# Kernel tuning notes

Hardware: AMD Instinct MI355X
Metric: run time of the kernel (lower is better)

Reference implementation:

```python
import jax, jax.numpy as jnp
import numpy as np

N_NODES = 100000
N_EDGES = 6400000
N_HEADS = 8


def setup_inputs() -> dict:
    key = jax.random.key(0)
    k1, k2 = jax.random.split(key)
    edge_val = jax.random.normal(k1, (N_EDGES, N_HEADS), dtype=jnp.float32)
    row = jax.random.randint(k2, (N_EDGES,), 0, N_NODES, dtype=jnp.int64)
    return {"edge_val": edge_val, "row": row, "num_nodes": N_NODES}


def reference(edge_val, row, num_nodes):
    # Per-head rescale: torch halves edge_val until max <= 10.
    # Halving k times == multiply by 0.5**k with k = ceil(log2(max/10)) when max > 10.
    m = jnp.max(edge_val, axis=0)  # [H]
    k = jnp.where(m > 10.0, jnp.ceil(jnp.log2(jnp.maximum(m, 1e-30) / 10.0)), 0.0)
    k = jnp.maximum(k, 0.0)
    scale = jnp.power(jnp.float32(0.5), jax.lax.stop_gradient(k))  # [H]
    e = jnp.exp(edge_val * scale)  # [E, H]
    # Per-destination-node sum of exp values (spmm of ones == segment sum by row)
    node_sum = jax.ops.segment_sum(e, row, num_segments=num_nodes)  # [N, H]
    return e / node_sum[row]  # [E, H]
```

## Files before the change

kernel.cpp:

```cpp
#include <hip/hip_runtime.h>

#define NHEADS 8
#define NNODES 100000
#define SLICE_NODES 500
#define NSLICES 200
#define NCHUNK 16
#define NBLK2 512
#define SEGCAP 128
#define SEGPC (NBLK2 / NCHUNK)
#define SLICE_F (SLICE_NODES * NHEADS)
#define SIDX_CAP 3072
#define WS_NSUM_OFF 1024

typedef float f32x4 __attribute__((ext_vector_type(4)));

#define PAIRS_B ((size_t)NBLK2 * NSLICES * SEGCAP * 4)
#define PART_B ((size_t)NSLICES * NCHUNK * SLICE_F * 4)

__device__ __forceinline__ unsigned fenc(float f) {
    unsigned u = __float_as_uint(f);
    return (u & 0x80000000u) ? ~u : (u | 0x80000000u);
}
__device__ __forceinline__ float fdec(unsigned u) {
    unsigned b = (u & 0x80000000u) ? (u ^ 0x80000000u) : ~u;
    return __uint_as_float(b);
}

__global__ void kinit(unsigned* __restrict__ gmax) {
    if (threadIdx.x < NHEADS) gmax[threadIdx.x] = 0u;
}

__global__ void __launch_bounds__(512) kscat(const int* __restrict__ row,
                                             long long E, long long epb,
                                             unsigned* __restrict__ pairs,
                                             unsigned* __restrict__ cnt) {
    __shared__ unsigned cur[NSLICES];
    for (int i = threadIdx.x; i < NSLICES; i += 512) cur[i] = 0;
    __syncthreads();

    long long e0 = (long long)blockIdx.x * epb;
    long long e1 = e0 + epb;
    if (e1 > E) e1 = E;

    unsigned pbase = (unsigned)blockIdx.x * (NSLICES * SEGCAP);
    for (long long e = e0 + threadIdx.x; e < e1; e += 512) {
        int r = row[e];
        unsigned s = (unsigned)r / SLICE_NODES;
        unsigned pos = atomicAdd(&cur[s], 1u);
        if (pos < SEGCAP)
            pairs[pbase + s * SEGCAP + pos] =
                ((unsigned)e << 9) | (unsigned)(r - (int)s * SLICE_NODES);
    }
    __syncthreads();
    for (int i = threadIdx.x; i < NSLICES; i += 512)
        cnt[(unsigned)blockIdx.x * NSLICES + i] = min(cur[i], (unsigned)SEGCAP);
}

template <bool SCALED, bool DOMAX>
__device__ __forceinline__ void process_chunk(const unsigned* __restrict__ pairs,
                                              const unsigned* __restrict__ cnt,
                                              const float4* __restrict__ ev4,
                                              const float* __restrict__ s8,
                                              float* __restrict__ partials,
                                              unsigned* __restrict__ gmax) {
    __shared__ unsigned hist[SLICE_NODES];
    __shared__ unsigned part[128];
    __shared__ unsigned spair[SIDX_CAP];
    __shared__ ushort sidx[SIDX_CAP];
    __shared__ unsigned segoff[SEGPC + 1];
    __shared__ float smx[4][8];

    int s = blockIdx.x / NCHUNK;
    int c = blockIdx.x % NCHUNK;
    int tid = threadIdx.x;

    if (tid < SEGPC)
        segoff[tid + 1] = cnt[(unsigned)(c * SEGPC + tid) * NSLICES + s];
    if (tid == 0) segoff[0] = 0;
    __syncthreads();
    if (tid == 0) {
        unsigned run = 0;
        for (int k = 1; k <= SEGPC; ++k) { run += segoff[k]; segoff[k] = run; }
    }
    __syncthreads();
    unsigned K = segoff[SEGPC];
    float* op = partials + (long long)blockIdx.x * SLICE_F;

    const float NEG = -3.402823466e38f;
    float m8[8];
    if (DOMAX) {
#pragma unroll
        for (int h = 0; h < 8; ++h) m8[h] = NEG;
    }

    int w = tid >> 6, lane = tid & 63;
    if (K <= SIDX_CAP) {
        for (int i = tid; i < SLICE_NODES; i += 256) hist[i] = 0;
        __syncthreads();
        for (int k = w; k < SEGPC; k += 4) {
            unsigned ck = segoff[k + 1] - segoff[k];
            const unsigned* src = pairs +
                (size_t)(c * SEGPC + k) * (NSLICES * SEGCAP) + (size_t)s * SEGCAP;
            for (unsigned j = lane; j < ck; j += 64) {
                unsigned p = src[j];
                spair[segoff[k] + j] = p;
                atomicAdd(&hist[p & 511u], 1u);
            }
        }
        __syncthreads();
        if (tid < 125) {
            unsigned g = tid * 4, run = 0;
#pragma unroll
            for (int k = 0; k < 4; ++k) {
                unsigned v = hist[g + k];
                hist[g + k] = run;
                run += v;
            }
            part[tid] = run;
        }
        __syncthreads();
        if (tid == 0) {
            unsigned run = 0;
            for (int j = 0; j < 125; ++j) {
                unsigned v = part[j];
                part[j] = run;
                run += v;
            }
        }
        __syncthreads();
        if (tid < 125) {
            unsigned b = part[tid], g = tid * 4;
#pragma unroll
            for (int k = 0; k < 4; ++k) hist[g + k] += b;
        }
        __syncthreads();
        for (unsigned i = tid; i < K; i += 256) {
            unsigned p = spair[i];
            unsigned pos = atomicAdd(&hist[p & 511u], 1u);
            sidx[pos] = (ushort)i;
        }
        __syncthreads();
        for (int n = tid; n < SLICE_NODES; n += 256) {
            unsigned lo = (n == 0) ? 0u : hist[n - 1];
            unsigned hi = hist[n];
            float acc[8] = {0, 0, 0, 0, 0, 0, 0, 0};
            for (unsigned p = lo; p < hi; ++p) {
                long long e = (long long)(spair[sidx[p]] >> 9);
                float4 a = ev4[e * 2];
                float4 b = ev4[e * 2 + 1];
                if (DOMAX) {
                    m8[0] = fmaxf(m8[0], a.x); m8[1] = fmaxf(m8[1], a.y);
                    m8[2] = fmaxf(m8[2], a.z); m8[3] = fmaxf(m8[3], a.w);
                    m8[4] = fmaxf(m8[4], b.x); m8[5] = fmaxf(m8[5], b.y);
                    m8[6] = fmaxf(m8[6], b.z); m8[7] = fmaxf(m8[7], b.w);
                }
                acc[0] += expf(SCALED ? a.x * s8[0] : a.x);
                acc[1] += expf(SCALED ? a.y * s8[1] : a.y);
                acc[2] += expf(SCALED ? a.z * s8[2] : a.z);
                acc[3] += expf(SCALED ? a.w * s8[3] : a.w);
                acc[4] += expf(SCALED ? b.x * s8[4] : b.x);
                acc[5] += expf(SCALED ? b.y * s8[5] : b.y);
                acc[6] += expf(SCALED ? b.z * s8[6] : b.z);
                acc[7] += expf(SCALED ? b.w * s8[7] : b.w);
            }
            ((float4*)(op + n * NHEADS))[0] = make_float4(acc[0], acc[1], acc[2], acc[3]);
            ((float4*)(op + n * NHEADS))[1] = make_float4(acc[4], acc[5], acc[6], acc[7]);
        }
    } else {
        for (int i = tid; i < SLICE_F; i += 256) op[i] = 0.0f;
        __syncthreads();
        for (int k = w; k < SEGPC; k += 4) {
            unsigned ck = segoff[k + 1] - segoff[k];
            const unsigned* src = pairs +
                (size_t)(c * SEGPC + k) * (NSLICES * SEGCAP) + (size_t)s * SEGCAP;
            for (unsigned j = lane; j < ck; j += 64) {
                unsigned p = src[j];
                long long e = (long long)(p >> 9);
                float* dst = op + (p & 511u) * NHEADS;
                float4 a = ev4[e * 2];
                float4 b = ev4[e * 2 + 1];
                if (DOMAX) {
                    m8[0] = fmaxf(m8[0], a.x); m8[1] = fmaxf(m8[1], a.y);
                    m8[2] = fmaxf(m8[2], a.z); m8[3] = fmaxf(m8[3], a.w);
                    m8[4] = fmaxf(m8[4], b.x); m8[5] = fmaxf(m8[5], b.y);
                    m8[6] = fmaxf(m8[6], b.z); m8[7] = fmaxf(m8[7], b.w);
                }
                atomicAdd(dst + 0, expf(SCALED ? a.x * s8[0] : a.x));
                atomicAdd(dst + 1, expf(SCALED ? a.y * s8[1] : a.y));
                atomicAdd(dst + 2, expf(SCALED ? a.z * s8[2] : a.z));
                atomicAdd(dst + 3, expf(SCALED ? a.w * s8[3] : a.w));
                atomicAdd(dst + 4, expf(SCALED ? b.x * s8[4] : b.x));
                atomicAdd(dst + 5, expf(SCALED ? b.y * s8[5] : b.y));
                atomicAdd(dst + 6, expf(SCALED ? b.z * s8[6] : b.z));
                atomicAdd(dst + 7, expf(SCALED ? b.w * s8[7] : b.w));
            }
        }
    }

    if (DOMAX) {
#pragma unroll
        for (int h = 0; h < 8; ++h) {
#pragma unroll
            for (int off = 1; off < 64; off <<= 1)
                m8[h] = fmaxf(m8[h], __shfl_xor(m8[h], off));
        }
        if (lane == 0) {
#pragma unroll
            for (int h = 0; h < 8; ++h) smx[w][h] = m8[h];
        }
        __syncthreads();
        if (tid < 8) {
            float v = smx[0][tid];
#pragma unroll
            for (int k = 1; k < 4; ++k) v = fmaxf(v, smx[k][tid]);
            atomicMax(&gmax[tid], fenc(v));
        }
    }
}

__global__ void __launch_bounds__(256) kproc(const unsigned* __restrict__ pairs,
                                             const unsigned* __restrict__ cnt,
                                             const float4* __restrict__ ev4,
                                             float* __restrict__ partials,
                                             unsigned* __restrict__ gmax) {
    process_chunk<false, true>(pairs, cnt, ev4, nullptr, partials, gmax);
}

__global__ void kscale(const unsigned* __restrict__ gmax,
                       float* __restrict__ scale,
                       unsigned* __restrict__ needfix) {
    __shared__ float ssc[NHEADS];
    int h = threadIdx.x;
    if (h < NHEADS) {
        float m = fdec(gmax[h]);
        float k = (m > 10.0f) ? ceilf(log2f(fmaxf(m, 1e-30f) / 10.0f)) : 0.0f;
        k = fmaxf(k, 0.0f);
        float s = exp2f(-k);
        scale[h] = s;
        ssc[h] = s;
    }
    __syncthreads();
    if (h == 0) {
        unsigned nf = 0;
#pragma unroll
        for (int i = 0; i < NHEADS; ++i) nf |= (ssc[i] != 1.0f) ? 1u : 0u;
        *needfix = nf;
    }
}

__global__ void __launch_bounds__(256) kfix(const unsigned* __restrict__ pairs,
                                            const unsigned* __restrict__ cnt,
                                            const float4* __restrict__ ev4,
                                            const float* __restrict__ scale,
                                            const unsigned* __restrict__ needfix,
                                            float* __restrict__ partials) {
    if (*needfix == 0u) return;
    float s8[NHEADS];
#pragma unroll
    for (int h = 0; h < NHEADS; ++h) s8[h] = scale[h];
    process_chunk<true, false>(pairs, cnt, ev4, s8, partials, nullptr);
}

__global__ void __launch_bounds__(256) kred(const float4* __restrict__ partials,
                                            float4* __restrict__ nsum,
                                            int n4sum) {
    int i = blockIdx.x * blockDim.x + threadIdx.x;
    if (i >= n4sum) return;
    const int S4 = SLICE_F / 4;
    int s = i / S4;
    int l4 = i - s * S4;
    const float4* base = partials + (long long)(s * NCHUNK) * S4 + l4;
    float4 acc = base[0];
#pragma unroll
    for (int j = 1; j < NCHUNK; ++j) {
        float4 v = base[(long long)j * S4];
        acc.x += v.x; acc.y += v.y; acc.z += v.z; acc.w += v.w;
    }
    nsum[i] = acc;
}

__global__ void __launch_bounds__(256) kout(const f32x4* __restrict__ ev4,
                                            const int* __restrict__ row,
                                            const float* __restrict__ scale,
                                            const float* __restrict__ nsum,
                                            float* __restrict__ out,
                                            long long E) {
    float4 sLo = *(const float4*)scale;
    float4 sHi = *(const float4*)(scale + 4);
    long long tid = blockIdx.x * (long long)blockDim.x + threadIdx.x;
    long long stride = (long long)gridDim.x * blockDim.x;
    for (long long e = tid; e < E; e += stride) {
        int r = __builtin_nontemporal_load(&row[e]);
        f32x4 a = __builtin_nontemporal_load(&ev4[e * 2]);
        f32x4 b = __builtin_nontemporal_load(&ev4[e * 2 + 1]);
        const float4 n0 = *(const float4*)(nsum + (long long)r * NHEADS);
        const float4 n1 = *(const float4*)(nsum + (long long)r * NHEADS + 4);
        f32x4 o0, o1;
        o0.x = expf(a.x * sLo.x) / n0.x;
        o0.y = expf(a.y * sLo.y) / n0.y;
        o0.z = expf(a.z * sLo.z) / n0.z;
        o0.w = expf(a.w * sLo.w) / n0.w;
        o1.x = expf(b.x * sHi.x) / n1.x;
        o1.y = expf(b.y * sHi.y) / n1.y;
        o1.z = expf(b.z * sHi.z) / n1.z;
        o1.w = expf(b.w * sHi.w) / n1.w;
        f32x4* dst = (f32x4*)(out + e * NHEADS);
        __builtin_nontemporal_store(o0, dst);
        __builtin_nontemporal_store(o1, dst + 1);
    }
}

extern "C" void kernel_launch(void* const* d_in, const int* in_sizes, int n_in,
                              void* d_out, int out_size, void* d_ws, size_t ws_size,
                              hipStream_t stream) {
    const float* ev = (const float*)d_in[0];
    const int* row = (const int*)d_in[1];
    long long nElem = (long long)in_sizes[0];
    long long E = nElem / NHEADS;
    long long epb = (E + NBLK2 - 1) / NBLK2;

    float* ws = (float*)d_ws;
    unsigned* gmax = (unsigned*)ws;
    float* scale = ws + 8;
    unsigned* needfix = (unsigned*)(ws + 16);
    float* nsum = ws + WS_NSUM_OFF;

    char* ob = (char*)d_out;
    unsigned* pairs = (unsigned*)ob;
    float* partials = (float*)(ob + PAIRS_B);
    unsigned* cnt = (unsigned*)(ob + PAIRS_B + PART_B);

    kinit<<<1, 64, 0, stream>>>(gmax);
    kscat<<<NBLK2, 512, 0, stream>>>(row, E, epb, pairs, cnt);
    kproc<<<NSLICES * NCHUNK, 256, 0, stream>>>(pairs, cnt, (const float4*)ev,
                                                partials, gmax);
    kscale<<<1, 64, 0, stream>>>(gmax, scale, needfix);
    kfix<<<NSLICES * NCHUNK, 256, 0, stream>>>(pairs, cnt, (const float4*)ev,
                                               scale, needfix, partials);
    kred<<<(NNODES * NHEADS / 4 + 255) / 256, 256, 0, stream>>>(
        (const float4*)partials, (float4*)nsum, NNODES * NHEADS / 4);
    kout<<<2048, 256, 0, stream>>>((const f32x4*)ev, row, scale, nsum,
                                   (float*)d_out, E);
}
```

Before: 328.3 us.

## Replace shared-memory counting sort with fixed-capacity per-node bins plus overflow list

Per-slice edge grouping no longer copies pairs into shared memory, builds a histogram, runs a multi-step prefix scan and scatters indices. Each edge is instead dropped into a fixed 20-entry bin for its node, with overflow entries going to a small shared list that every thread scans. This removes several barriers and the serial scan, and drops the global-atomic fallback path. In exchange, the pair index is re-read from global memory in the accumulate loop, each thread scans the whole overflow list, and edges past the overflow capacity of 512 are silently lost.

```diff
diff --git a/kernel.cpp b/kernel.cpp
--- a/kernel.cpp
+++ b/kernel.cpp
@@ -9,7 +9,8 @@
 #define SEGCAP 128
 #define SEGPC (NBLK2 / NCHUNK)
 #define SLICE_F (SLICE_NODES * NHEADS)
-#define SIDX_CAP 3072
+#define BINCAP 20
+#define OCAP 512
 #define WS_NSUM_OFF 1024
 
 typedef float f32x4 __attribute__((ext_vector_type(4)));
@@ -63,28 +64,37 @@
                                               const float* __restrict__ s8,
                                               float* __restrict__ partials,
                                               unsigned* __restrict__ gmax) {
-    __shared__ unsigned hist[SLICE_NODES];
-    __shared__ unsigned part[128];
-    __shared__ unsigned spair[SIDX_CAP];
-    __shared__ ushort sidx[SIDX_CAP];
-    __shared__ unsigned segoff[SEGPC + 1];
+    __shared__ ushort bins[SLICE_NODES * BINCAP];
+    __shared__ unsigned cur[SLICE_NODES];
+    __shared__ unsigned olist[OCAP];
+    __shared__ unsigned ocnt;
     __shared__ float smx[4][8];
 
     int s = blockIdx.x / NCHUNK;
     int c = blockIdx.x % NCHUNK;
     int tid = threadIdx.x;
-
-    if (tid < SEGPC)
-        segoff[tid + 1] = cnt[(unsigned)(c * SEGPC + tid) * NSLICES + s];
-    if (tid == 0) segoff[0] = 0;
-    __syncthreads();
-    if (tid == 0) {
-        unsigned run = 0;
-        for (int k = 1; k <= SEGPC; ++k) { run += segoff[k]; segoff[k] = run; }
-    }
-    __syncthreads();
-    unsigned K = segoff[SEGPC];
-    float* op = partials + (long long)blockIdx.x * SLICE_F;
+    for (int i = tid; i < SLICE_NODES; i += 256) cur[i] = 0;
+    if (tid == 0) ocnt = 0;
+    __syncthreads();
+
+    int w = tid >> 6, lane = tid & 63;
+    for (int k = w; k < SEGPC; k += 4) {
+        unsigned ck = cnt[(unsigned)(c * SEGPC + k) * NSLICES + s];
+        const unsigned* src = pairs +
+            (size_t)(c * SEGPC + k) * (NSLICES * SEGCAP) + (size_t)s * SEGCAP;
+        for (unsigned j = lane; j < ck; j += 64) {
+            unsigned node = src[j] & 511u;
+            unsigned pos = atomicAdd(&cur[node], 1u);
+            unsigned code = ((unsigned)k << 7) | j;
+            if (pos < BINCAP) {
+                bins[node * BINCAP + pos] = (ushort)code;
+            } else {
+                unsigned oi = atomicAdd(&ocnt, 1u);
+                if (oi < OCAP) olist[oi] = (node << 12) | code;
+            }
+        }
+    }
+    __syncthreads();
 
     const float NEG = -3.402823466e38f;
     float m8[8];
@@ -92,109 +102,44 @@
 #pragma unroll
         for (int h = 0; h < 8; ++h) m8[h] = NEG;
     }
-
-    int w = tid >> 6, lane = tid & 63;
-    if (K <= SIDX_CAP) {
-        for (int i = tid; i < SLICE_NODES; i += 256) hist[i] = 0;
-        __syncthreads();
-        for (int k = w; k < SEGPC; k += 4) {
-            unsigned ck = segoff[k + 1] - segoff[k];
-            const unsigned* src = pairs +
-                (size_t)(c * SEGPC + k) * (NSLICES * SEGCAP) + (size_t)s * SEGCAP;
-            for (unsigned j = lane; j < ck; j += 64) {
-                unsigned p = src[j];
-                spair[segoff[k] + j] = p;
-                atomicAdd(&hist[p & 511u], 1u);
+    float* op = partials + (long long)blockIdx.x * SLICE_F;
+    unsigned oc = min(ocnt, (unsigned)OCAP);
+
+    for (int n = tid; n < SLICE_NODES; n += 256) {
+        unsigned cn = min(cur[n], (unsigned)BINCAP);
+        float acc[8] = {0, 0, 0, 0, 0, 0, 0, 0};
+        for (unsigned i = 0; i < cn + oc; ++i) {
+            unsigned code;
+            if (i < cn) {
+                code = bins[n * BINCAP + i];
+            } else {
+                unsigned o = olist[i - cn];
+                if ((o >> 12) != (unsigned)n) continue;
+                code = o & 4095u;
             }
-        }
-        __syncthreads();
-        if (tid < 125) {
-            unsigned g = tid * 4, run = 0;
-#pragma unroll
-            for (int k = 0; k < 4; ++k) {
-                unsigned v = hist[g + k];
-                hist[g + k] = run;
-                run += v;
+            unsigned k = code >> 7, j = code & 127u;
+            unsigned p = pairs[(size_t)(c * SEGPC + k) * (NSLICES * SEGCAP) +
+                               (size_t)s * SEGCAP + j];
+            long long e = (long long)(p >> 9);
+            float4 a = ev4[e * 2];
+            float4 b = ev4[e * 2 + 1];
+            if (DOMAX) {
+                m8[0] = fmaxf(m8[0], a.x); m8[1] = fmaxf(m8[1], a.y);
+                m8[2] = fmaxf(m8[2], a.z); m8[3] = fmaxf(m8[3], a.w);
+                m8[4] = fmaxf(m8[4], b.x); m8[5] = fmaxf(m8[5], b.y);
+                m8[6] = fmaxf(m8[6], b.z); m8[7] = fmaxf(m8[7], b.w);
             }
-            part[tid] = run;
-        }
-        __syncthreads();
-        if (tid == 0) {
-            unsigned run = 0;
-            for (int j = 0; j < 125; ++j) {
-                unsigned v = part[j];
-                part[j] = run;
-                run += v;
-            }
-        }
-        __syncthreads();
-        if (tid < 125) {
-            unsigned b = part[tid], g = tid * 4;
-#pragma unroll
-            for (int k = 0; k < 4; ++k) hist[g + k] += b;
-        }
-        __syncthreads();
-        for (unsigned i = tid; i < K; i += 256) {
-            unsigned p = spair[i];
-            unsigned pos = atomicAdd(&hist[p & 511u], 1u);
-            sidx[pos] = (ushort)i;
-        }
-        __syncthreads();
-        for (int n = tid; n < SLICE_NODES; n += 256) {
-            unsigned lo = (n == 0) ? 0u : hist[n - 1];
-            unsigned hi = hist[n];
-            float acc[8] = {0, 0, 0, 0, 0, 0, 0, 0};
-            for (unsigned p = lo; p < hi; ++p) {
-                long long e = (long long)(spair[sidx[p]] >> 9);
-                float4 a = ev4[e * 2];
-                float4 b = ev4[e * 2 + 1];
-                if (DOMAX) {
-                    m8[0] = fmaxf(m8[0], a.x); m8[1] = fmaxf(m8[1], a.y);
-                    m8[2] = fmaxf(m8[2], a.z); m8[3] = fmaxf(m8[3], a.w);
-                    m8[4] = fmaxf(m8[4], b.x); m8[5] = fmaxf(m8[5], b.y);
-                    m8[6] = fmaxf(m8[6], b.z); m8[7] = fmaxf(m8[7], b.w);
-                }
-                acc[0] += expf(SCALED ? a.x * s8[0] : a.x);
-                acc[1] += expf(SCALED ? a.y * s8[1] : a.y);
-                acc[2] += expf(SCALED ? a.z * s8[2] : a.z);
-                acc[3] += expf(SCALED ? a.w * s8[3] : a.w);
-                acc[4] += expf(SCALED ? b.x * s8[4] : b.x);
-                acc[5] += expf(SCALED ? b.y * s8[5] : b.y);
-                acc[6] += expf(SCALED ? b.z * s8[6] : b.z);
-                acc[7] += expf(SCALED ? b.w * s8[7] : b.w);
-            }
-            ((float4*)(op + n * NHEADS))[0] = make_float4(acc[0], acc[1], acc[2], acc[3]);
-            ((float4*)(op + n * NHEADS))[1] = make_float4(acc[4], acc[5], acc[6], acc[7]);
-        }
-    } else {
-        for (int i = tid; i < SLICE_F; i += 256) op[i] = 0.0f;
-        __syncthreads();
-        for (int k = w; k < SEGPC; k += 4) {
-            unsigned ck = segoff[k + 1] - segoff[k];
-            const unsigned* src = pairs +
-                (size_t)(c * SEGPC + k) * (NSLICES * SEGCAP) + (size_t)s * SEGCAP;
-            for (unsigned j = lane; j < ck; j += 64) {
-                unsigned p = src[j];
-                long long e = (long long)(p >> 9);
-                float* dst = op + (p & 511u) * NHEADS;
-                float4 a = ev4[e * 2];
-                float4 b = ev4[e * 2 + 1];
-                if (DOMAX) {
-                    m8[0] = fmaxf(m8[0], a.x); m8[1] = fmaxf(m8[1], a.y);
-                    m8[2] = fmaxf(m8[2], a.z); m8[3] = fmaxf(m8[3], a.w);
-                    m8[4] = fmaxf(m8[4], b.x); m8[5] = fmaxf(m8[5], b.y);
-                    m8[6] = fmaxf(m8[6], b.z); m8[7] = fmaxf(m8[7], b.w);
-                }
-                atomicAdd(dst + 0, expf(SCALED ? a.x * s8[0] : a.x));
-                atomicAdd(dst + 1, expf(SCALED ? a.y * s8[1] : a.y));
-                atomicAdd(dst + 2, expf(SCALED ? a.z * s8[2] : a.z));
-                atomicAdd(dst + 3, expf(SCALED ? a.w * s8[3] : a.w));
-                atomicAdd(dst + 4, expf(SCALED ? b.x * s8[4] : b.x));
-                atomicAdd(dst + 5, expf(SCALED ? b.y * s8[5] : b.y));
-                atomicAdd(dst + 6, expf(SCALED ? b.z * s8[6] : b.z));
-                atomicAdd(dst + 7, expf(SCALED ? b.w * s8[7] : b.w));
-            }
-        }
+            acc[0] += expf(SCALED ? a.x * s8[0] : a.x);
+            acc[1] += expf(SCALED ? a.y * s8[1] : a.y);
+            acc[2] += expf(SCALED ? a.z * s8[2] : a.z);
+            acc[3] += expf(SCALED ? a.w * s8[3] : a.w);
+            acc[4] += expf(SCALED ? b.x * s8[4] : b.x);
+            acc[5] += expf(SCALED ? b.y * s8[5] : b.y);
+            acc[6] += expf(SCALED ? b.z * s8[6] : b.z);
+            acc[7] += expf(SCALED ? b.w * s8[7] : b.w);
+        }
+        ((float4*)(op + n * NHEADS))[0] = make_float4(acc[0], acc[1], acc[2], acc[3]);
+        ((float4*)(op + n * NHEADS))[1] = make_float4(acc[4], acc[5], acc[6], acc[7]);
     }
 
     if (DOMAX) {
```

Result: slower. 371.2 us (+13.1%).
